# Kernel tuning notes

Measured on AMD Instinct MI355X. Metric: run time of the kernel, lower is better.

The kernel has to match this reference:

```python
import jax, jax.numpy as jnp
import numpy as np

N_NODES = 100000
N_EDGES = 3200000
N_GRAPHS = 1000
HID = 64
L = 4  # num_unit


def setup_inputs() -> dict:
    key = jax.random.key(0)
    ks = jax.random.split(key, 16)
    x = jax.random.normal(ks[0], (N_NODES, 4), dtype=jnp.float32)
    edge_index = jax.random.randint(ks[1], (2, N_EDGES), 0, N_NODES, dtype=jnp.int64)
    edge_attr = jax.random.uniform(ks[2], (N_EDGES,), dtype=jnp.float32)
    batch = jnp.sort(jax.random.randint(ks[3], (N_NODES,), 0, N_GRAPHS, dtype=jnp.int64))
    s = 1.0 / np.sqrt(HID)
    inp = {
        'x': x, 'edge_index': edge_index, 'edge_attr': edge_attr, 'batch': batch,
        'emb_w': jax.random.normal(ks[4], (4, HID), jnp.float32) * 0.5,
        'emb_b': jnp.zeros((HID,), jnp.float32),
        'conv_w1': jax.random.normal(ks[5], (L, HID, HID), jnp.float32) * s,
        'conv_b1': jnp.zeros((L, HID), jnp.float32),
        'conv_w2': jax.random.normal(ks[6], (L, HID, HID), jnp.float32) * s,
        'conv_w3': jax.random.normal(ks[7], (L, HID, HID), jnp.float32) * s,
        'conv_b3': jnp.zeros((L, HID), jnp.float32),
        'lin1_w': jax.random.normal(ks[8], (HID, HID), jnp.float32) * s,
        'lin1_b': jnp.zeros((HID,), jnp.float32),
        'lin2_w': jax.random.normal(ks[9], (HID, 3), jnp.float32) * s,
        'lin2_b': jnp.zeros((3,), jnp.float32),
    }
    return inp


def _forward(x, edge_index, edge_attr, batch,
             emb_w, emb_b, conv_w1, conv_b1, conv_w2, conv_w3, conv_b3,
             lin1_w, lin1_b, lin2_w, lin2_b):
    src, dst = edge_index[0], edge_index[1]
    ew = edge_attr[:, None]  # [E,1]
    h = x @ emb_w + emb_b  # node_emb; dropout omitted (eval mode)
    for l in range(conv_w1.shape[0]):
        # LEConv: out_i = sum_{j->i} w_ji * (lin1(x_j) - lin2(x_i)) + lin3(x_i)
        a = h @ conv_w1[l] + conv_b1[l]
        b = h @ conv_w2[l]  # no bias
        msg = (a[src] - b[dst]) * ew  # [E, HID]
        agg = jax.ops.segment_sum(msg, dst, num_segments=h.shape[0])
        h = jax.nn.relu(agg + h @ conv_w3[l] + conv_b3[l])
    # global mean pool over graphs
    sums = jax.ops.segment_sum(h, batch, num_segments=N_GRAPHS)
    cnt = jax.ops.segment_sum(jnp.ones((h.shape[0],), h.dtype), batch, num_segments=N_GRAPHS)
    graph_x = sums / jnp.maximum(cnt, 1.0)[:, None]
    pred = jax.nn.relu(graph_x @ lin1_w + lin1_b) @ lin2_w + lin2_b
    return pred


def reference(x, edge_index, edge_attr, batch, emb_w, emb_b,
              conv_w1, conv_b1, conv_w2, conv_w3, conv_b3,
              lin1_w, lin1_b, lin2_w, lin2_b):
    return _forward(x, edge_index, edge_attr, batch, emb_w, emb_b,
                    conv_w1, conv_b1, conv_w2, conv_w3, conv_b3,
                    lin1_w, lin1_b, lin2_w, lin2_b)
```

## Files before the change

### kernel.cpp

```cpp
#include <hip/hip_runtime.h>

#define N_NODES 100000
#define N_EDGES 3200000
#define N_GRAPHS 1000
#define NLAYER 4
#define NB 782
#define BBITS 7
#define EPB2 2048
#define G1 1563
#define GH 782
#define PCAP 6144

typedef __attribute__((ext_vector_type(8))) short bf16x8;
typedef __attribute__((ext_vector_type(4))) float f32x4;

static __device__ __forceinline__ unsigned f2bf(float f) {
  unsigned u = __float_as_uint(f);
  return (u + 0x7fffu + ((u >> 16) & 1u)) >> 16;
}
static __device__ __forceinline__ float bf2f_lo(unsigned u) {
  return __uint_as_float(u << 16);
}
static __device__ __forceinline__ float bf2f_hi(unsigned u) {
  return __uint_as_float(u & 0xffff0000u);
}

__global__ __launch_bounds__(256) void zero_kernel(int* __restrict__ p, int n)
{
  int i = blockIdx.x * 256 + threadIdx.x;
  if (i < n) p[i] = 0;
}

__global__ __launch_bounds__(256) void embed_kernel(
    const float* __restrict__ x, const float* __restrict__ emb_w,
    const float* __restrict__ emb_b, unsigned short* __restrict__ h_bf)
{
  int t = blockIdx.x * 256 + threadIdx.x;
  if (t >= N_NODES * 64) return;
  int c = t & 63, v = t >> 6;
  float4 xv = ((const float4*)x)[v];
  float acc = emb_b[c];
  acc = fmaf(xv.x, emb_w[0 * 64 + c], acc);
  acc = fmaf(xv.y, emb_w[1 * 64 + c], acc);
  acc = fmaf(xv.z, emb_w[2 * 64 + c], acc);
  acc = fmaf(xv.w, emb_w[3 * 64 + c], acc);
  h_bf[t] = (unsigned short)f2bf(acc);
}

__global__ __launch_bounds__(256) void hist1_kernel(
    const int* __restrict__ ei, int* __restrict__ tots)
{
  __shared__ unsigned hist[NB];
  for (int i = threadIdx.x; i < NB; i += 256) hist[i] = 0;
  __syncthreads();
  int base = blockIdx.x * 4096;
#pragma unroll
  for (int i = 0; i < 16; ++i) {
    int e = base + i * 256 + threadIdx.x;
    if (e < N_EDGES) atomicAdd(&hist[((unsigned)ei[N_EDGES + e]) >> BBITS], 1u);
  }
  __syncthreads();
  for (int i = threadIdx.x; i < NB; i += 256) {
    unsigned c = hist[i];
    if (c) atomicAdd(&tots[i], (int)c);
  }
}

__global__ __launch_bounds__(1024) void scan1_kernel(
    const int* __restrict__ tots, int* __restrict__ bb, int* __restrict__ gcur)
{
  __shared__ int s[1024];
  int t = threadIdx.x;
  int x = (t < NB) ? tots[t] : 0;
  s[t] = x;
  __syncthreads();
  for (int off = 1; off < 1024; off <<= 1) {
    int y = (t >= off) ? s[t - off] : 0;
    __syncthreads();
    s[t] += y;
    __syncthreads();
  }
  if (t < NB) {
    int ex = s[t] - x;
    bb[t] = ex;
    gcur[t] = ex;
  }
  if (t == 0) bb[NB] = N_EDGES;
}

__global__ __launch_bounds__(256) void bscatter2_kernel(
    const int* __restrict__ ei, const float* __restrict__ ea,
    int* __restrict__ gcur, int2* __restrict__ tmp)
{
  __shared__ unsigned hist[NB];
  __shared__ int dif[NB];
  __shared__ int2 stage[EPB2];
  __shared__ unsigned short bid[EPB2];
  __shared__ int sbuf[256];
  __shared__ int carry;
  int tid = threadIdx.x;
  int base = blockIdx.x * EPB2;

  for (int i = tid; i < NB; i += 256) hist[i] = 0;
  if (tid == 0) carry = 0;
  __syncthreads();

#pragma unroll
  for (int i = 0; i < 8; ++i) {
    int e = base + i * 256 + tid;
    if (e < N_EDGES) atomicAdd(&hist[((unsigned)ei[N_EDGES + e]) >> BBITS], 1u);
  }
  __syncthreads();

  for (int b = tid; b < NB; b += 256) {
    int c = (int)hist[b];
    dif[b] = c ? atomicAdd(&gcur[b], c) : 0;
  }
  __syncthreads();

  for (int c0 = 0; c0 < NB; c0 += 256) {
    int g = c0 + tid;
    int v = (g < NB) ? (int)hist[g] : 0;
    sbuf[tid] = v;
    __syncthreads();
    for (int off = 1; off < 256; off <<= 1) {
      int y = (tid >= off) ? sbuf[tid - off] : 0;
      __syncthreads();
      sbuf[tid] += y;
      __syncthreads();
    }
    if (g < NB) {
      int ex = carry + sbuf[tid] - v;
      hist[g] = (unsigned)ex;
      dif[g] -= ex;
    }
    __syncthreads();
    if (tid == 0) carry += sbuf[255];
    __syncthreads();
  }

#pragma unroll
  for (int i = 0; i < 8; ++i) {
    int e = base + i * 256 + tid;
    if (e < N_EDGES) {
      int d = ei[N_EDGES + e];
      unsigned bkt = ((unsigned)d) >> BBITS;
      unsigned lp = atomicAdd(&hist[bkt], 1u);
      stage[lp] = make_int2(ei[e] | ((d & 127) << 17), __float_as_int(ea[e]));
      bid[lp] = (unsigned short)bkt;
    }
  }
  __syncthreads();

  int nE = min(EPB2, N_EDGES - base);
  for (int i = tid; i < nE; i += 256) {
    int bkt = (int)bid[i];
    tmp[dif[bkt] + i] = stage[i];
  }
}

__global__ __launch_bounds__(256) void bucket_sort2_kernel(
    const int* __restrict__ bb, const int2* __restrict__ tmp,
    unsigned* __restrict__ csr, int* __restrict__ row_off, float* __restrict__ degw)
{
  int j = blockIdx.x;
  int b0 = bb[j], b1 = bb[j + 1];
  int nE = b1 - b0;
  __shared__ unsigned hist[128];
  __shared__ float dws[128];
  __shared__ int scanbuf[256];
  __shared__ unsigned cur[128];
  __shared__ unsigned short perm[PCAP];
  int t = threadIdx.x;
  if (t < 128) { hist[t] = 0; dws[t] = 0.f; }
  __syncthreads();
  for (int i = t; i < nE; i += 256) {
    int2 r = tmp[b0 + i];
    int bin = ((unsigned)r.x) >> 17;
    atomicAdd(&hist[bin], 1u);
    atomicAdd(&dws[bin], __int_as_float(r.y));
  }
  __syncthreads();
  int v = (t < 128) ? (int)hist[t] : 0;
  scanbuf[t] = v;
  __syncthreads();
  for (int off = 1; off < 256; off <<= 1) {
    int y = (t >= off) ? scanbuf[t - off] : 0;
    __syncthreads();
    scanbuf[t] += y;
    __syncthreads();
  }
  int myexcl = scanbuf[t] - v;
  if (t < 128) {
    cur[t] = (unsigned)myexcl;
    int vnode = (j << BBITS) + t;
    if (vnode < N_NODES) {
      row_off[vnode] = b0 + myexcl;
      degw[vnode] = dws[t];
    }
  }
  if (j == NB - 1 && t == 0) row_off[N_NODES] = N_EDGES;
  __syncthreads();

  if (nE <= PCAP) {
    for (int i = t; i < nE; i += 256) {
      int2 r = tmp[b0 + i];
      int bin = ((unsigned)r.x) >> 17;
      unsigned p = atomicAdd(&cur[bin], 1u);
      perm[p] = (unsigned short)i;
    }
    __syncthreads();
    for (int q = t; q < nE; q += 256) {
      int2 r = tmp[b0 + (int)perm[q]];
      unsigned q15 = (unsigned)(__int_as_float(r.y) * 32768.0f);
      csr[b0 + q] = ((unsigned)r.x & 0x1FFFFu) | (q15 << 17);
    }
  } else {
    for (int i = t; i < nE; i += 256) {
      int2 r = tmp[b0 + i];
      int bin = ((unsigned)r.x) >> 17;
      unsigned p = atomicAdd(&cur[bin], 1u);
      unsigned q15 = (unsigned)(__int_as_float(r.y) * 32768.0f);
      csr[b0 + (int)p] = ((unsigned)r.x & 0x1FFFFu) | (q15 << 17);
    }
  }
}

__global__ __launch_bounds__(256) void dhist_kernel(
    const int* __restrict__ row_off, int* __restrict__ dhist)
{
  __shared__ unsigned h[256];
  int t = threadIdx.x;
  h[t] = 0;
  __syncthreads();
  int v0 = (blockIdx.x * 256 + t) * 4;
#pragma unroll
  for (int k = 0; k < 4; ++k) {
    int v = v0 + k;
    if (v < N_NODES) {
      int d = row_off[v + 1] - row_off[v];
      atomicAdd(&h[min(d, 255)], 1u);
    }
  }
  __syncthreads();
  unsigned c = h[t];
  if (c) atomicAdd(&dhist[t], (int)c);
}

__global__ __launch_bounds__(256) void dscan_kernel(
    const int* __restrict__ dhist, int* __restrict__ dcur)
{
  __shared__ int s[256];
  int t = threadIdx.x;
  int v = dhist[t];
  s[t] = v;
  __syncthreads();
  for (int off = 1; off < 256; off <<= 1) {
    int y = (t >= off) ? s[t - off] : 0;
    __syncthreads();
    s[t] += y;
    __syncthreads();
  }
  dcur[t] = s[t] - v;
}

__global__ __launch_bounds__(256) void dperm_kernel(
    const int* __restrict__ row_off, int* __restrict__ dcur,
    int* __restrict__ nodeperm)
{
  __shared__ unsigned h[256];
  __shared__ unsigned lcur[256];
  int t = threadIdx.x;
  h[t] = 0;
  __syncthreads();
  int v0 = (blockIdx.x * 256 + t) * 4;
  int dloc[4];
#pragma unroll
  for (int k = 0; k < 4; ++k) {
    int v = v0 + k;
    dloc[k] = -1;
    if (v < N_NODES) {
      int d = min(row_off[v + 1] - row_off[v], 255);
      dloc[k] = d;
      atomicAdd(&h[d], 1u);
    }
  }
  __syncthreads();
  unsigned c = h[t];
  unsigned gb = c ? (unsigned)atomicAdd(&dcur[t], (int)c) : 0u;
  lcur[t] = gb;
  __syncthreads();
#pragma unroll
  for (int k = 0; k < 4; ++k) {
    if (dloc[k] >= 0) {
      unsigned p = atomicAdd(&lcur[dloc[k]], 1u);
      nodeperm[p] = v0 + k;
    }
  }
}

__global__ __launch_bounds__(256) void wswz_kernel(
    const float* __restrict__ cw1, const float* __restrict__ cw2,
    const float* __restrict__ cw3, unsigned* __restrict__ wswz)
{
  int l = blockIdx.x;
  const float* w1 = cw1 + l * 4096;
  const float* w2 = cw2 + l * 4096;
  const float* w3 = cw3 + l * 4096;
  unsigned* outp = wswz + l * 6144;
  int tid = threadIdx.x;
  int n = tid & 63;
  int gofs = tid >> 6;
  for (int it = 0; it < 24; ++it) {
    int g = it * 4 + gofs;
    int m = g >> 5;
    int kp = g & 31;
    int k = kp * 2;
    const float* W = (m == 0) ? w2 : (m == 1) ? w3 : w1;
    unsigned lo = f2bf(W[k * 64 + n]);
    unsigned hi = f2bf(W[(k + 1) * 64 + n]);
    int c = k >> 5;
    int kk = k & 31;
    int lane = ((kk >> 3) << 4) | (n & 15);
    int j2 = (kk & 7) >> 1;
    int t = n >> 4;
    outp[(((m * 2 + c) * 4 + t) << 8) | (lane << 2) | j2] = lo | (hi << 16);
  }
}

__global__ __launch_bounds__(256) void matvec3_mfma_kernel(
    const unsigned short* __restrict__ h_bf,
    const unsigned* __restrict__ wz,
    const float* __restrict__ b1, const float* __restrict__ b3,
    const float* __restrict__ degw,
    unsigned short* __restrict__ a_bf, unsigned short* __restrict__ cc_bf)
{
  int gw = (blockIdx.x * 256 + threadIdx.x) >> 6;
  int lane = threadIdx.x & 63;
  int quad = lane >> 4;
  int col = lane & 15;
  int nb = gw * 16;
  if (nb >= N_NODES) return;

  int arow = nb + col;
  if (arow >= N_NODES) arow = N_NODES - 1;
  const bf16x8* ap = (const bf16x8*)(h_bf + (size_t)arow * 64 + quad * 8);
  bf16x8 af0 = ap[0];
  bf16x8 af1 = ap[4];

  float dwr[4];
#pragma unroll
  for (int r = 0; r < 4; ++r) {
    int row = nb + quad * 4 + r;
    dwr[r] = degw[row < N_NODES ? row : 0];
  }

#pragma unroll
  for (int t = 0; t < 4; ++t) {
    const bf16x8* b20 = (const bf16x8*)&wz[((0 * 4 + t) << 8) + lane * 4];
    const bf16x8* b21 = (const bf16x8*)&wz[((1 * 4 + t) << 8) + lane * 4];
    const bf16x8* b30 = (const bf16x8*)&wz[((2 * 4 + t) << 8) + lane * 4];
    const bf16x8* b31 = (const bf16x8*)&wz[((3 * 4 + t) << 8) + lane * 4];
    const bf16x8* b10 = (const bf16x8*)&wz[((4 * 4 + t) << 8) + lane * 4];
    const bf16x8* b11 = (const bf16x8*)&wz[((5 * 4 + t) << 8) + lane * 4];

    f32x4 z = {0.f, 0.f, 0.f, 0.f};
    f32x4 acc2 = __builtin_amdgcn_mfma_f32_16x16x32_bf16(af0, *b20, z, 0, 0, 0);
    acc2 = __builtin_amdgcn_mfma_f32_16x16x32_bf16(af1, *b21, acc2, 0, 0, 0);
    f32x4 cc;
#pragma unroll
    for (int r = 0; r < 4; ++r) cc[r] = -dwr[r] * acc2[r];
    cc = __builtin_amdgcn_mfma_f32_16x16x32_bf16(af0, *b30, cc, 0, 0, 0);
    cc = __builtin_amdgcn_mfma_f32_16x16x32_bf16(af1, *b31, cc, 0, 0, 0);
    float bb3 = b3[t * 16 + col];
#pragma unroll
    for (int r = 0; r < 4; ++r) {
      int row = nb + quad * 4 + r;
      if (row < N_NODES)
        cc_bf[(size_t)row * 64 + t * 16 + col] = (unsigned short)f2bf(cc[r] + bb3);
    }

    float bb1 = b1[t * 16 + col];
    f32x4 a1 = {bb1, bb1, bb1, bb1};
    a1 = __builtin_amdgcn_mfma_f32_16x16x32_bf16(af0, *b10, a1, 0, 0, 0);
    a1 = __builtin_amdgcn_mfma_f32_16x16x32_bf16(af1, *b11, a1, 0, 0, 0);
#pragma unroll
    for (int r = 0; r < 4; ++r) {
      int row = nb + quad * 4 + r;
      if (row < N_NODES)
        a_bf[(size_t)row * 64 + t * 16 + col] = (unsigned short)f2bf(a1[r]);
    }
  }
}

__global__ __launch_bounds__(256) void agg_kernel(
    const uint2* __restrict__ a2, const uint2* __restrict__ cc2,
    const int* __restrict__ row_off, const unsigned* __restrict__ csr,
    const int* __restrict__ nodeperm,
    float4* __restrict__ h4, unsigned short* __restrict__ h_bf, int write_h)
{
  int wave = (blockIdx.x * 256 + threadIdx.x) >> 6;
  int lane = threadIdx.x & 63;
  int sg = lane >> 4;
  int li = lane & 15;
  int lsel = (lane & 48) << 2;
  int vslot = wave * 4 + sg;
  bool valid = vslot < N_NODES;
  int v = nodeperm[valid ? vslot : N_NODES - 1];
  int base = row_off[v];
  int ecnt = valid ? (row_off[v + 1] - base) : 0;

  float4 acc = make_float4(0.f, 0.f, 0.f, 0.f);
  if (valid) {
    uint2 cu = cc2[(size_t)v * 16 + li];
    acc.x = bf2f_lo(cu.x);
    acc.y = bf2f_hi(cu.x);
    acc.z = bf2f_lo(cu.y);
    acc.w = bf2f_hi(cu.y);
  }
  const uint2* ap = a2 + li;

  int full = ecnt & ~15;
  int c0 = 0;
  for (; c0 < full; c0 += 16) {
    int er = (int)csr[base + c0 + li];
#pragma unroll
    for (int j = 0; j < 16; ++j) {
      unsigned r = (unsigned)__builtin_amdgcn_ds_bpermute(lsel | (j << 2), er);
      int s = (int)(r & 0x1FFFFu);
      float w = (float)(r >> 17) * (1.0f / 32768.0f);
      uint2 u = ap[(size_t)s * 16];
      acc.x = fmaf(w, bf2f_lo(u.x), acc.x);
      acc.y = fmaf(w, bf2f_hi(u.x), acc.y);
      acc.z = fmaf(w, bf2f_lo(u.y), acc.z);
      acc.w = fmaf(w, bf2f_hi(u.y), acc.w);
    }
  }
  int rem = ecnt - full;
  if (rem > 0) {
    int idx = c0 + li;
    int er = (idx < ecnt) ? (int)csr[base + idx] : 0;
    for (int j = 0; j < rem; ++j) {
      unsigned r = (unsigned)__builtin_amdgcn_ds_bpermute(lsel | (j << 2), er);
      int s = (int)(r & 0x1FFFFu);
      float w = (float)(r >> 17) * (1.0f / 32768.0f);
      uint2 u = ap[(size_t)s * 16];
      acc.x = fmaf(w, bf2f_lo(u.x), acc.x);
      acc.y = fmaf(w, bf2f_hi(u.x), acc.y);
      acc.z = fmaf(w, bf2f_lo(u.y), acc.z);
      acc.w = fmaf(w, bf2f_hi(u.y), acc.w);
    }
  }
  if (valid) {
    acc.x = fmaxf(acc.x, 0.f);
    acc.y = fmaxf(acc.y, 0.f);
    acc.z = fmaxf(acc.z, 0.f);
    acc.w = fmaxf(acc.w, 0.f);
    if (write_h) h4[(size_t)v * 16 + li] = acc;
    uint2 p;
    p.x = f2bf(acc.x) | (f2bf(acc.y) << 16);
    p.y = f2bf(acc.z) | (f2bf(acc.w) << 16);
    ((uint2*)h_bf)[(size_t)v * 16 + li] = p;
  }
}

__global__ __launch_bounds__(256) void head_kernel(
    const float* __restrict__ h, const int* __restrict__ batch,
    const float* __restrict__ l1w, const float* __restrict__ l1b,
    const float* __restrict__ l2w, const float* __restrict__ l2b,
    float* __restrict__ out)
{
  int g = (blockIdx.x * 256 + threadIdx.x) >> 6;
  int lane = threadIdx.x & 63;
  if (g >= N_GRAPHS) return;
  int lo = 0, hi = N_NODES;
  while (lo < hi) { int mid = (lo + hi) >> 1; if (batch[mid] < g) lo = mid + 1; else hi = mid; }
  int start = lo;
  hi = N_NODES;
  while (lo < hi) { int mid = (lo + hi) >> 1; if (batch[mid] < g + 1) lo = mid + 1; else hi = mid; }
  int end = lo;

  float sum = 0.f;
  for (int v = start; v < end; ++v) sum += h[(size_t)v * 64 + lane];
  float cntf = (float)(end - start);
  float gx = sum / fmaxf(cntf, 1.f);

  float acc = l1b[lane];
  for (int k = 0; k < 64; ++k) {
    float gxk = __shfl(gx, k);
    acc = fmaf(gxk, l1w[k * 64 + lane], acc);
  }
  float t = fmaxf(acc, 0.f);
  float p0 = t * l2w[lane * 3 + 0];
  float p1 = t * l2w[lane * 3 + 1];
  float p2 = t * l2w[lane * 3 + 2];
  for (int off = 32; off > 0; off >>= 1) {
    p0 += __shfl_down(p0, off);
    p1 += __shfl_down(p1, off);
    p2 += __shfl_down(p2, off);
  }
  if (lane == 0) {
    out[g * 3 + 0] = p0 + l2b[0];
    out[g * 3 + 1] = p1 + l2b[1];
    out[g * 3 + 2] = p2 + l2b[2];
  }
}

extern "C" void kernel_launch(void* const* d_in, const int* in_sizes, int n_in,
                              void* d_out, int out_size, void* d_ws, size_t ws_size,
                              hipStream_t stream)
{
  (void)in_sizes; (void)n_in; (void)out_size; (void)ws_size;
  const float* x     = (const float*)d_in[0];
  const int*   ei    = (const int*)d_in[1];
  const float* ea    = (const float*)d_in[2];
  const int*   batch = (const int*)d_in[3];
  const float* emb_w = (const float*)d_in[4];
  const float* emb_b = (const float*)d_in[5];
  const float* cw1   = (const float*)d_in[6];
  const float* cb1   = (const float*)d_in[7];
  const float* cw2   = (const float*)d_in[8];
  const float* cw3   = (const float*)d_in[9];
  const float* cb3   = (const float*)d_in[10];
  const float* l1w   = (const float*)d_in[11];
  const float* l1b   = (const float*)d_in[12];
  const float* l2w   = (const float*)d_in[13];
  const float* l2b   = (const float*)d_in[14];
  float* out = (float*)d_out;

  char* wsb = (char*)d_ws;
  size_t off = 0;
  auto alloc = [&](size_t bytes) {
    char* p = wsb + off;
    off = (off + bytes + 255) & ~(size_t)255;
    return p;
  };
  float* h       = (float*)alloc(sizeof(float) * (size_t)N_NODES * 64);
  unsigned short* h_bf = (unsigned short*)alloc(sizeof(short) * (size_t)N_NODES * 64);
  unsigned short* a_bf = (unsigned short*)alloc(sizeof(short) * (size_t)N_NODES * 64);
  unsigned short* cc_bf = (unsigned short*)alloc(sizeof(short) * (size_t)N_NODES * 64);
  unsigned* csr  = (unsigned*)alloc(sizeof(unsigned) * (size_t)N_EDGES);
  int*   row_off = (int*)alloc(sizeof(int) * (N_NODES + 1));
  float* degw    = (float*)alloc(sizeof(float) * N_NODES);
  int*   nodeperm= (int*)alloc(sizeof(int) * N_NODES);
  int*   tots    = (int*)alloc(sizeof(int) * NB);
  int*   dhist_g = (int*)alloc(sizeof(int) * 256);
  int*   bb      = (int*)alloc(sizeof(int) * (NB + 1));
  int*   gcur    = (int*)alloc(sizeof(int) * NB);
  int*   dcur    = (int*)alloc(sizeof(int) * 256);
  unsigned* wswz = (unsigned*)alloc(sizeof(unsigned) * NLAYER * 6144);
  int2* tmp = (int2*)h;

  zero_kernel<<<(NB + 255) / 256, 256, 0, stream>>>(tots, NB);
  zero_kernel<<<1, 256, 0, stream>>>(dhist_g, 256);

  embed_kernel<<<(N_NODES * 64 + 255) / 256, 256, 0, stream>>>(x, emb_w, emb_b, h_bf);
  wswz_kernel<<<NLAYER, 256, 0, stream>>>(cw1, cw2, cw3, wswz);
  hist1_kernel<<<GH, 256, 0, stream>>>(ei, tots);
  scan1_kernel<<<1, 1024, 0, stream>>>(tots, bb, gcur);
  bscatter2_kernel<<<G1, 256, 0, stream>>>(ei, ea, gcur, tmp);
  bucket_sort2_kernel<<<NB, 256, 0, stream>>>(bb, tmp, csr, row_off, degw);
  dhist_kernel<<<98, 256, 0, stream>>>(row_off, dhist_g);
  dscan_kernel<<<1, 256, 0, stream>>>(dhist_g, dcur);
  dperm_kernel<<<98, 256, 0, stream>>>(row_off, dcur, nodeperm);

  int agg_blocks = (N_NODES + 15) / 16;
  int mv_blocks = (N_NODES / 16 + 3) / 4 + 1;
  for (int l = 0; l < NLAYER; ++l) {
    matvec3_mfma_kernel<<<mv_blocks, 256, 0, stream>>>(
        h_bf, wswz + l * 6144, cb1 + l * 64, cb3 + l * 64, degw, a_bf, cc_bf);
    agg_kernel<<<agg_blocks, 256, 0, stream>>>(
        (const uint2*)a_bf, (const uint2*)cc_bf, row_off, csr, nodeperm, (float4*)h,
        h_bf, (l == NLAYER - 1) ? 1 : 0);
  }

  head_kernel<<<(N_GRAPHS * 64 + 255) / 256, 256, 0, stream>>>(
      h, batch, l1w, l1b, l2w, l2b, out);
}
```

Before: 591.5 us.

## Simplify bucket scatter: direct global writes, larger per-block tiles, shuffle scan

The bucket scatter kernel no longer stages edges in shared memory or runs a block-wide prefix scan. Each block now handles twice as many edges, keeps destinations in registers, reserves global offsets per bucket, and writes each edge straight to its slot through an atomic cursor in shared memory. This removes the in-block scan, its many barriers, and the staging pass, at the cost of less coalesced scattered global writes. The single-block scan1 kernel is also rewritten to use wavefront shuffles in place of a 1024-entry shared-memory scan.

```diff
diff --git a/kernel.cpp b/kernel.cpp
--- a/kernel.cpp
+++ b/kernel.cpp
@@ -6,8 +6,8 @@
 #define NLAYER 4
 #define NB 782
 #define BBITS 7
-#define EPB2 2048
-#define G1 1563
+#define EPB2 4096
+#define G1 782
 #define GH 782
 #define PCAP 6144
 
@@ -69,93 +69,73 @@
 __global__ __launch_bounds__(1024) void scan1_kernel(
     const int* __restrict__ tots, int* __restrict__ bb, int* __restrict__ gcur)
 {
-  __shared__ int s[1024];
+  __shared__ int wsum[16];
   int t = threadIdx.x;
+  int lane = t & 63;
+  int w = t >> 6;
   int x = (t < NB) ? tots[t] : 0;
-  s[t] = x;
-  __syncthreads();
-  for (int off = 1; off < 1024; off <<= 1) {
-    int y = (t >= off) ? s[t - off] : 0;
-    __syncthreads();
-    s[t] += y;
-    __syncthreads();
-  }
+  int s = x;
+  for (int off = 1; off < 64; off <<= 1) {
+    int y = __shfl_up(s, off);
+    if (lane >= off) s += y;
+  }
+  if (lane == 63) wsum[w] = s;
+  __syncthreads();
+  if (w == 0 && lane < 16) {
+    int v = wsum[lane];
+    int ss = v;
+    for (int off = 1; off < 16; off <<= 1) {
+      int y = __shfl_up(ss, off);
+      if (lane >= off) ss += y;
+    }
+    wsum[lane] = ss - v;
+  }
+  __syncthreads();
+  int ex = wsum[w] + s - x;
   if (t < NB) {
-    int ex = s[t] - x;
     bb[t] = ex;
     gcur[t] = ex;
   }
   if (t == 0) bb[NB] = N_EDGES;
 }
 
-__global__ __launch_bounds__(256) void bscatter2_kernel(
+__global__ __launch_bounds__(256) void bscatter3_kernel(
     const int* __restrict__ ei, const float* __restrict__ ea,
     int* __restrict__ gcur, int2* __restrict__ tmp)
 {
   __shared__ unsigned hist[NB];
-  __shared__ int dif[NB];
-  __shared__ int2 stage[EPB2];
-  __shared__ unsigned short bid[EPB2];
-  __shared__ int sbuf[256];
-  __shared__ int carry;
   int tid = threadIdx.x;
   int base = blockIdx.x * EPB2;
-
   for (int i = tid; i < NB; i += 256) hist[i] = 0;
-  if (tid == 0) carry = 0;
-  __syncthreads();
-
-#pragma unroll
-  for (int i = 0; i < 8; ++i) {
+  __syncthreads();
+
+  int dreg[16];
+#pragma unroll
+  for (int i = 0; i < 16; ++i) {
     int e = base + i * 256 + tid;
-    if (e < N_EDGES) atomicAdd(&hist[((unsigned)ei[N_EDGES + e]) >> BBITS], 1u);
-  }
-  __syncthreads();
-
-  for (int b = tid; b < NB; b += 256) {
-    int c = (int)hist[b];
-    dif[b] = c ? atomicAdd(&gcur[b], c) : 0;
-  }
-  __syncthreads();
-
-  for (int c0 = 0; c0 < NB; c0 += 256) {
-    int g = c0 + tid;
-    int v = (g < NB) ? (int)hist[g] : 0;
-    sbuf[tid] = v;
-    __syncthreads();
-    for (int off = 1; off < 256; off <<= 1) {
-      int y = (tid >= off) ? sbuf[tid - off] : 0;
-      __syncthreads();
-      sbuf[tid] += y;
-      __syncthreads();
-    }
-    if (g < NB) {
-      int ex = carry + sbuf[tid] - v;
-      hist[g] = (unsigned)ex;
-      dif[g] -= ex;
-    }
-    __syncthreads();
-    if (tid == 0) carry += sbuf[255];
-    __syncthreads();
-  }
-
-#pragma unroll
-  for (int i = 0; i < 8; ++i) {
-    int e = base + i * 256 + tid;
+    dreg[i] = -1;
     if (e < N_EDGES) {
       int d = ei[N_EDGES + e];
-      unsigned bkt = ((unsigned)d) >> BBITS;
-      unsigned lp = atomicAdd(&hist[bkt], 1u);
-      stage[lp] = make_int2(ei[e] | ((d & 127) << 17), __float_as_int(ea[e]));
-      bid[lp] = (unsigned short)bkt;
-    }
-  }
-  __syncthreads();
-
-  int nE = min(EPB2, N_EDGES - base);
-  for (int i = tid; i < nE; i += 256) {
-    int bkt = (int)bid[i];
-    tmp[dif[bkt] + i] = stage[i];
+      dreg[i] = d;
+      atomicAdd(&hist[((unsigned)d) >> BBITS], 1u);
+    }
+  }
+  __syncthreads();
+
+  for (int b = tid; b < NB; b += 256) {
+    unsigned c = hist[b];
+    hist[b] = c ? (unsigned)atomicAdd(&gcur[b], (int)c) : 0u;
+  }
+  __syncthreads();
+
+#pragma unroll
+  for (int i = 0; i < 16; ++i) {
+    int e = base + i * 256 + tid;
+    int d = dreg[i];
+    if (d >= 0) {
+      unsigned p = atomicAdd(&hist[((unsigned)d) >> BBITS], 1u);
+      tmp[p] = make_int2(ei[e] | ((d & 127) << 17), __float_as_int(ea[e]));
+    }
   }
 }
 
@@ -558,7 +538,7 @@
   wswz_kernel<<<NLAYER, 256, 0, stream>>>(cw1, cw2, cw3, wswz);
   hist1_kernel<<<GH, 256, 0, stream>>>(ei, tots);
   scan1_kernel<<<1, 1024, 0, stream>>>(tots, bb, gcur);
-  bscatter2_kernel<<<G1, 256, 0, stream>>>(ei, ea, gcur, tmp);
+  bscatter3_kernel<<<G1, 256, 0, stream>>>(ei, ea, gcur, tmp);
   bucket_sort2_kernel<<<NB, 256, 0, stream>>>(bb, tmp, csr, row_off, degw);
   dhist_kernel<<<98, 256, 0, stream>>>(row_off, dhist_g);
   dscan_kernel<<<1, 256, 0, stream>>>(dhist_g, dcur);
```

Result: no change. 595.2 us (+0.6%).
